# Kernel optimization log

Hardware: AMD Instinct MI355X
Metric: run time of the kernel (lower is better)

The kernel has to match this reference:

```python
import jax, jax.numpy as jnp
import numpy as np

B, IN_C, OUT_C, K, H, W = 8, 256, 256, 3, 128, 128
EPS = 1e-8
ACT_SCALE = np.sqrt(2.0).astype(np.float32)


def setup_inputs() -> dict:
    key = jax.random.key(0)
    k1, k2, k3 = jax.random.split(key, 3)
    return {
        "x": jax.random.normal(k1, (B, IN_C, H, W), dtype=jnp.float32),
        "code": jax.random.normal(k2, (B, IN_C), dtype=jnp.float32),
        "weight": jax.random.normal(k3, (OUT_C, IN_C, K, K), dtype=jnp.float32),
        "bias": jnp.zeros((OUT_C,), dtype=jnp.float32),
    }


def reference(x, code, weight, bias):
    b, in_c, h, w = x.shape
    out_c, _, k, _ = weight.shape
    wscale = np.float32(1.0 / np.sqrt(k * k * in_c))
    # Same memory reinterpretation as torch .view: (out_c,in_c,k,k) -> (1,k,k,in_c,out_c)
    wv = (weight * wscale).reshape(1, k, k, in_c, out_c)
    # modulate per-sample by code over input channels
    wm = wv * code[:, None, None, :, None]            # [b,k,k,in_c,out_c]
    # demodulate: norm over (k,k,in_c) per (b,out_c)
    norm = jnp.sqrt(jnp.sum(wm * wm, axis=(1, 2, 3)) + EPS)  # [b,out_c]
    wm = wm / norm[:, None, None, None, :]
    # reshape to grouped-conv kernel [b*out_c, in_c, k, k]
    wk = jnp.transpose(wm, (0, 4, 3, 1, 2)).reshape(b * out_c, in_c, k, k)
    xg = x.reshape(1, b * in_c, h, w)
    y = jax.lax.conv_general_dilated(
        xg, wk, window_strides=(1, 1),
        padding=[(k // 2, k // 2), (k // 2, k // 2)],
        feature_group_count=b,
        dimension_numbers=("NCHW", "OIHW", "NCHW"))
    y = y.reshape(b, out_c, h, w) + bias[None, :, None, None]
    # LeakyReLU(0.2) * sqrt(2)
    return jnp.where(y >= 0, y, 0.2 * y) * ACT_SCALE
```

## Files before the change

kernel.cpp:

```cpp
#include <hip/hip_runtime.h>
#include <hip/hip_bf16.h>


typedef __attribute__((ext_vector_type(8))) short short8;
typedef __attribute__((ext_vector_type(4))) float floatx4;
typedef __attribute__((ext_vector_type(4))) unsigned short ushort4_t;
typedef __bf16 bf16x8 __attribute__((ext_vector_type(8)));

#define B_    8
#define IC_   256
#define OC_   256
#define HW_   128
#define PIX_  (HW_*HW_)
#define RTOT  2304
#define WSCALE (1.0f/48.0f)
#define STRX  40
#define STRW  104

static __device__ __forceinline__ floatx4 mfma_bf16(short8 a, short8 b, floatx4 c) {
  return __builtin_amdgcn_mfma_f32_16x16x32_bf16(
      __builtin_bit_cast(bf16x8, a), __builtin_bit_cast(bf16x8, b), c, 0, 0, 0);
}

static __device__ __forceinline__ unsigned short f2bf(float f) {
  unsigned int u = __builtin_bit_cast(unsigned int, f);
  return (unsigned short)(u >> 16) + (unsigned short)((u >> 15) & 1u);
}

__global__ __launch_bounds__(256) void k_zero(float* __restrict__ p, int n) {
  int i = blockIdx.x * 256 + threadIdx.x;
  if (i < n) p[i] = 0.f;
}

__global__ __launch_bounds__(256) void k_transpose(const float* __restrict__ x,
                                                   unsigned short* __restrict__ Xt,
                                                   int b0) {
  __shared__ unsigned short t[64][66];
  const int tid = threadIdx.x;
  const int p0 = blockIdx.x * 64, ic0 = blockIdx.y * 64, bz = blockIdx.z;
  const float* xb = x + (size_t)(b0 + bz) * IC_ * PIX_;
  unsigned short* xtb = Xt + (size_t)bz * PIX_ * IC_;

  const int c2 = tid & 15, r2 = tid >> 4;
#pragma unroll
  for (int jr = 0; jr < 4; ++jr) {
    const int row = r2 + jr * 16;
    floatx4 f = *(const floatx4*)(&xb[(size_t)(ic0 + row) * PIX_ + p0 + 4 * c2]);
    t[row][4 * c2 + 0] = f2bf(f[0]);
    t[row][4 * c2 + 1] = f2bf(f[1]);
    t[row][4 * c2 + 2] = f2bf(f[2]);
    t[row][4 * c2 + 3] = f2bf(f[3]);
  }
  __syncthreads();
#pragma unroll
  for (int jj = 0; jj < 4; ++jj) {
    const int px = r2 + jj * 16;
    ushort4_t v = { t[4 * c2 + 0][px], t[4 * c2 + 1][px],
                    t[4 * c2 + 2][px], t[4 * c2 + 3][px] };
    *(ushort4_t*)(&xtb[(size_t)(p0 + px) * IC_ + ic0 + 4 * c2]) = v;
  }
}

__global__ __launch_bounds__(256) void k_norm(const float* __restrict__ Wraw,
                                              const float* __restrict__ code,
                                              float* __restrict__ norm2) {
  const int tap = blockIdx.x % 9, b = blockIdx.x / 9;
  const int oc = threadIdx.x;
  __shared__ float cs[IC_];
  cs[oc] = code[b * IC_ + oc];
  __syncthreads();
  float s = 0.f;
#pragma unroll 8
  for (int ic = 0; ic < IC_; ++ic) {
    float v = Wraw[(size_t)(tap * IC_ + ic) * OC_ + oc] * cs[ic];
    s += v * v;
  }
  atomicAdd(&norm2[b * OC_ + oc], s * (WSCALE * WSCALE));
}

__global__ __launch_bounds__(256) void k_modw(const float* __restrict__ Wraw,
                                              const float* __restrict__ code,
                                              const float* __restrict__ norm2,
                                              unsigned short* __restrict__ Wt) {
  const int idx = blockIdx.x * 256 + threadIdx.x;
  const int r  = idx % RTOT;
  const int t2 = idx / RTOT;
  const int oc = t2 & 255;
  const int b  = t2 >> 8;
  const int ic = r & 255;
  const float w  = Wraw[(size_t)r * OC_ + oc];
  const float cd = code[b * IC_ + ic];
  const float rn = rsqrtf(norm2[b * OC_ + oc] + 1e-8f);
  Wt[idx] = f2bf(w * cd * WSCALE * rn);
}

__global__ __launch_bounds__(256, 2) void k_conv(const unsigned short* __restrict__ Xt,
                                                 const unsigned short* __restrict__ Wt,
                                                 const float* __restrict__ bias,
                                                 float* __restrict__ out,
                                                 int b0) {
  __shared__ __align__(16) unsigned short Wl[2][128 * STRW];
  __shared__ __align__(16) unsigned short Xl[2][130 * STRX];

  const int tid  = threadIdx.x;
  const int lane = tid & 63;
  const int wv   = tid >> 6;
  const int wm   = wv & 1;
  const int wn   = wv >> 1;
  const int l15  = lane & 15;
  const int k0   = (lane >> 4) * 8;

  const int py = blockIdx.x, ot = blockIdx.y, bz = blockIdx.z;
  const int b  = b0 + bz;

  const unsigned short* Wtp = Wt + (size_t)(b * OC_ + ot * 128) * RTOT;
  const unsigned short* Xtp = Xt + (size_t)bz * PIX_ * IC_;

  const int xc   = 1 + (tid >> 1);
  const int xh   = tid & 1;
  const int wocr = tid >> 1;

  const int lo = (py > 0) ? py - 1 : 0;
  const int hi = (py < HW_ - 1) ? py + 1 : HW_ - 1;
  const int NS = (hi - lo + 1) * 8;

  const floatx4 zz = {0.f, 0.f, 0.f, 0.f};
  floatx4 acc[4][4];
#pragma unroll
  for (int i = 0; i < 4; ++i)
#pragma unroll
    for (int j = 0; j < 4; ++j) acc[i][j] = zz;

  if (tid < 128) {
    const int bi = tid >> 6, rr = tid & 63;
    const int c = (rr < 32) ? 0 : 129;
    Xl[bi][c * STRX + (rr & 31)] = 0;
  }

  short8 xr0, xr1, wr0, wr1, wr2, wr3, wr4, wr5;

#define CLOAD(s_) do {                                                           \
    const int iy_   = lo + ((s_) >> 3);                                          \
    const int icc_  = (s_) & 7;                                                  \
    const int tapb_ = (iy_ - py + 1) * 3;                                        \
    const unsigned short* xs_ =                                                  \
        Xtp + (size_t)(iy_ * HW_ + xc - 1) * IC_ + icc_ * 32 + xh * 16;          \
    xr0 = *(const short8*)(xs_);                                                 \
    xr1 = *(const short8*)(xs_ + 8);                                             \
    const unsigned short* ws_ =                                                  \
        Wtp + (size_t)wocr * RTOT + (size_t)tapb_ * IC_ + icc_ * 32 + xh * 16;   \
    wr0 = *(const short8*)(ws_);                                                 \
    wr1 = *(const short8*)(ws_ + 8);                                             \
    wr2 = *(const short8*)(ws_ + IC_);                                           \
    wr3 = *(const short8*)(ws_ + IC_ + 8);                                       \
    wr4 = *(const short8*)(ws_ + 2 * IC_);                                       \
    wr5 = *(const short8*)(ws_ + 2 * IC_ + 8);                                   \
  } while (0)

#define DSW(b_) do {                                                             \
    unsigned short* xd_ = &Xl[b_][xc * STRX + xh * 16];                          \
    *(short8*)(xd_)     = xr0;                                                   \
    *(short8*)(xd_ + 8) = xr1;                                                   \
    unsigned short* wd_ = &Wl[b_][wocr * STRW + xh * 16];                        \
    *(short8*)(wd_)      = wr0;                                                  \
    *(short8*)(wd_ + 8)  = wr1;                                                  \
    *(short8*)(wd_ + 32) = wr2;                                                  \
    *(short8*)(wd_ + 40) = wr3;                                                  \
    *(short8*)(wd_ + 64) = wr4;                                                  \
    *(short8*)(wd_ + 72) = wr5;                                                  \
  } while (0)

  CLOAD(0);
  DSW(0);
  __syncthreads();

  for (int s = 0; s < NS; ++s) {
    const int nb = s & 1;
    if (s + 1 < NS) CLOAD(s + 1);

#pragma unroll
    for (int kx = 0; kx < 3; ++kx) {
      short8 af[4], bfr[4];
#pragma unroll
      for (int i = 0; i < 4; ++i)
        af[i] = *(const short8*)(&Wl[nb][(wm * 64 + i * 16 + l15) * STRW + kx * 32 + k0]);
#pragma unroll
      for (int j = 0; j < 4; ++j)
        bfr[j] = *(const short8*)(&Xl[nb][(wn * 64 + j * 16 + l15 + kx) * STRX + k0]);
#pragma unroll
      for (int i = 0; i < 4; ++i)
#pragma unroll
        for (int j = 0; j < 4; ++j)
          acc[i][j] = mfma_bf16(af[i], bfr[j], acc[i][j]);
    }

    if (s + 1 < NS) DSW(nb ^ 1);
    __syncthreads();
  }

#undef CLOAD
#undef DSW

  const int row0 = (lane >> 4) * 4;
#pragma unroll
  for (int i = 0; i < 4; ++i) {
#pragma unroll
    for (int p = 0; p < 4; ++p) {
      const int oc = ot * 128 + wm * 64 + i * 16 + row0 + p;
      const float bvf = bias[oc];
#pragma unroll
      for (int j = 0; j < 4; ++j) {
        const int px = wn * 64 + j * 16 + l15;
        float v = acc[i][j][p] + bvf;
        v = (v >= 0.f ? v : 0.2f * v) * 1.41421356237f;
        out[((size_t)(b * OC_ + oc) * HW_ + py) * HW_ + px] = v;
      }
    }
  }
}

extern "C" void kernel_launch(void* const* d_in, const int* in_sizes, int n_in,
                              void* d_out, int out_size, void* d_ws, size_t ws_size,
                              hipStream_t stream) {
  const float* x    = (const float*)d_in[0];
  const float* code = (const float*)d_in[1];
  const float* wgt  = (const float*)d_in[2];
  const float* bias = (const float*)d_in[3];

  const size_t WT_BYTES = (size_t)B_ * OC_ * RTOT * 2;
  const size_t N2_BYTES = (size_t)B_ * OC_ * 4;
  const size_t XT_OFF   = WT_BYTES + N2_BYTES;
  const size_t XB_BYTES = (size_t)PIX_ * IC_ * 2;

  unsigned short* Wt = (unsigned short*)d_ws;
  float* norm2       = (float*)((char*)d_ws + WT_BYTES);
  unsigned short* Xt = (unsigned short*)((char*)d_ws + XT_OFF);

  int bc = 8;
  while (bc > 1 && XT_OFF + (size_t)bc * XB_BYTES > ws_size) bc >>= 1;

  k_zero<<<(B_ * OC_ + 255) / 256, 256, 0, stream>>>(norm2, B_ * OC_);
  k_norm<<<B_ * 9, 256, 0, stream>>>(wgt, code, norm2);
  k_modw<<<(B_ * OC_ * RTOT) / 256, 256, 0, stream>>>(wgt, code, norm2, Wt);
  for (int b0 = 0; b0 < B_; b0 += bc) {
    k_transpose<<<dim3(PIX_ / 64, IC_ / 64, bc), 256, 0, stream>>>(x, Xt, b0);
    k_conv<<<dim3(HW_, 2, bc), 256, 0, stream>>>(Xt, Wt, bias, (float*)d_out, b0);
  }
}
```

Baseline: 426.9 us.

## Swizzle LDS tiles, remap workgroup order, and raise MFMA wave priority

The padded LDS strides in the conv kernel are replaced by XOR-swizzled 32-element rows, and the weight tile is split per kx tap. The goal is to avoid LDS bank conflicts while using less shared memory than padding does. Workgroup IDs are also remapped in an interleaved order across groups of eight, likely to spread work across XCDs and improve L2 locality. The MFMA section now runs under s_setprio, and the transpose kernel's LDS writes are vectorised. Together these bring extra index arithmetic and some scheduling risk.

```diff
diff --git a/kernel.cpp b/kernel.cpp
--- a/kernel.cpp
+++ b/kernel.cpp
@@ -14,8 +14,8 @@
 #define PIX_  (HW_*HW_)
 #define RTOT  2304
 #define WSCALE (1.0f/48.0f)
-#define STRX  40
-#define STRW  104
+
+#define SWZ(row) ((((row) ^ ((row) >> 2)) & 3) << 3)
 
 static __device__ __forceinline__ floatx4 mfma_bf16(short8 a, short8 b, floatx4 c) {
   return __builtin_amdgcn_mfma_f32_16x16x32_bf16(
@@ -46,10 +46,8 @@
   for (int jr = 0; jr < 4; ++jr) {
     const int row = r2 + jr * 16;
     floatx4 f = *(const floatx4*)(&xb[(size_t)(ic0 + row) * PIX_ + p0 + 4 * c2]);
-    t[row][4 * c2 + 0] = f2bf(f[0]);
-    t[row][4 * c2 + 1] = f2bf(f[1]);
-    t[row][4 * c2 + 2] = f2bf(f[2]);
-    t[row][4 * c2 + 3] = f2bf(f[3]);
+    ushort4_t w = { f2bf(f[0]), f2bf(f[1]), f2bf(f[2]), f2bf(f[3]) };
+    *(ushort4_t*)(&t[row][4 * c2]) = w;
   }
   __syncthreads();
 #pragma unroll
@@ -99,8 +97,8 @@
                                                  const float* __restrict__ bias,
                                                  float* __restrict__ out,
                                                  int b0) {
-  __shared__ __align__(16) unsigned short Wl[2][128 * STRW];
-  __shared__ __align__(16) unsigned short Xl[2][130 * STRX];
+  __shared__ __align__(16) unsigned short Wl[2][3][128 * 32];
+  __shared__ __align__(16) unsigned short Xl[2][130 * 32];
 
   const int tid  = threadIdx.x;
   const int lane = tid & 63;
@@ -110,7 +108,11 @@
   const int l15  = lane & 15;
   const int k0   = (lane >> 4) * 8;
 
-  const int py = blockIdx.x, ot = blockIdx.y, bz = blockIdx.z;
+  const int nwg  = (int)(gridDim.x * gridDim.y * gridDim.z);
+  const int q    = nwg >> 3;
+  const int flat = (int)(blockIdx.x + gridDim.x * (blockIdx.y + gridDim.y * blockIdx.z));
+  const int nf   = (flat & 7) * q + (flat >> 3);
+  const int py = nf & 127, ot = (nf >> 7) & 1, bz = nf >> 8;
   const int b  = b0 + bz;
 
   const unsigned short* Wtp = Wt + (size_t)(b * OC_ + ot * 128) * RTOT;
@@ -119,6 +121,11 @@
   const int xc   = 1 + (tid >> 1);
   const int xh   = tid & 1;
   const int wocr = tid >> 1;
+  const int sST  = SWZ(wocr);
+  const int sXC  = SWZ(xc);
+
+  const int sA  = SWZ(l15);
+  const int sB0 = SWZ(l15 + 0), sB1 = SWZ(l15 + 1), sB2 = SWZ(l15 + 2);
 
   const int lo = (py > 0) ? py - 1 : 0;
   const int hi = (py < HW_ - 1) ? py + 1 : HW_ - 1;
@@ -133,8 +140,8 @@
 
   if (tid < 128) {
     const int bi = tid >> 6, rr = tid & 63;
-    const int c = (rr < 32) ? 0 : 129;
-    Xl[bi][c * STRX + (rr & 31)] = 0;
+    const int r = (rr < 32) ? 0 : 129;
+    Xl[bi][r * 32 + (rr & 31)] = 0;
   }
 
   short8 xr0, xr1, wr0, wr1, wr2, wr3, wr4, wr5;
@@ -158,16 +165,18 @@
   } while (0)
 
 #define DSW(b_) do {                                                             \
-    unsigned short* xd_ = &Xl[b_][xc * STRX + xh * 16];                          \
-    *(short8*)(xd_)     = xr0;                                                   \
-    *(short8*)(xd_ + 8) = xr1;                                                   \
-    unsigned short* wd_ = &Wl[b_][wocr * STRW + xh * 16];                        \
-    *(short8*)(wd_)      = wr0;                                                  \
-    *(short8*)(wd_ + 8)  = wr1;                                                  \
-    *(short8*)(wd_ + 32) = wr2;                                                  \
-    *(short8*)(wd_ + 40) = wr3;                                                  \
-    *(short8*)(wd_ + 64) = wr4;                                                  \
-    *(short8*)(wd_ + 72) = wr5;                                                  \
+    unsigned short* xd_ = &Xl[b_][xc * 32];                                      \
+    *(short8*)(&xd_[(xh * 16)     ^ sXC]) = xr0;                                 \
+    *(short8*)(&xd_[(xh * 16 + 8) ^ sXC]) = xr1;                                 \
+    unsigned short* wd0_ = &Wl[b_][0][wocr * 32];                                \
+    unsigned short* wd1_ = &Wl[b_][1][wocr * 32];                                \
+    unsigned short* wd2_ = &Wl[b_][2][wocr * 32];                                \
+    *(short8*)(&wd0_[(xh * 16)     ^ sST]) = wr0;                                \
+    *(short8*)(&wd0_[(xh * 16 + 8) ^ sST]) = wr1;                                \
+    *(short8*)(&wd1_[(xh * 16)     ^ sST]) = wr2;                                \
+    *(short8*)(&wd1_[(xh * 16 + 8) ^ sST]) = wr3;                                \
+    *(short8*)(&wd2_[(xh * 16)     ^ sST]) = wr4;                                \
+    *(short8*)(&wd2_[(xh * 16 + 8) ^ sST]) = wr5;                                \
   } while (0)
 
   CLOAD(0);
@@ -178,21 +187,24 @@
     const int nb = s & 1;
     if (s + 1 < NS) CLOAD(s + 1);
 
+    __builtin_amdgcn_s_setprio(1);
 #pragma unroll
     for (int kx = 0; kx < 3; ++kx) {
+      const int sB = (kx == 0) ? sB0 : (kx == 1) ? sB1 : sB2;
       short8 af[4], bfr[4];
 #pragma unroll
       for (int i = 0; i < 4; ++i)
-        af[i] = *(const short8*)(&Wl[nb][(wm * 64 + i * 16 + l15) * STRW + kx * 32 + k0]);
+        af[i] = *(const short8*)(&Wl[nb][kx][(wm * 64 + i * 16 + l15) * 32 + (k0 ^ sA)]);
 #pragma unroll
       for (int j = 0; j < 4; ++j)
-        bfr[j] = *(const short8*)(&Xl[nb][(wn * 64 + j * 16 + l15 + kx) * STRX + k0]);
+        bfr[j] = *(const short8*)(&Xl[nb][(wn * 64 + j * 16 + l15 + kx) * 32 + (k0 ^ sB)]);
 #pragma unroll
       for (int i = 0; i < 4; ++i)
 #pragma unroll
         for (int j = 0; j < 4; ++j)
           acc[i][j] = mfma_bf16(af[i], bfr[j], acc[i][j]);
     }
+    __builtin_amdgcn_s_setprio(0);
 
     if (s + 1 < NS) DSW(nb ^ 1);
     __syncthreads();
```

After: 424.8 us. No clear change (-0.5%).
